# Optimization experiments

Hardware: AMD Instinct MI355X
Metric: run time of the kernel (lower is better)

Reference implementation:

```python
import jax, jax.numpy as jnp
import numpy as np

N, FIN, H, C, D = 50000, 128, 4, 64, 4
E = 800000


def leaky_relu(x, slope):
    return jnp.where(x >= 0, x, slope * x)


def gat_layer(x, src, dst, W, A, att_src, att_dst, bias):
    # x: [N, Fin]; W: [Fin, H*C]; A: [Fin, H*D]; att_*: [H, D]; bias: [C]
    n = x.shape[0]
    h = (x @ W).reshape(n, H, -1)          # [N, H, C] message features
    a = (x @ A).reshape(n, H, -1)          # [N, H, D] attention features
    alpha_src = jnp.einsum('nhd,hd->nh', a, att_src)   # [N, H]
    alpha_dst = jnp.einsum('nhd,hd->nh', a, att_dst)   # [N, H]
    e = leaky_relu(alpha_src[src] + alpha_dst[dst], 0.2)  # [E, H]
    # edge softmax over incoming edges of each destination node
    m = jax.ops.segment_max(e, dst, num_segments=n)       # [N, H]
    ex = jnp.exp(e - m[dst])                               # [E, H]
    denom = jax.ops.segment_sum(ex, dst, num_segments=n)  # [N, H]
    w = ex / denom[dst]                                    # [E, H]
    msg = h[src] * w[..., None]                            # [E, H, C]
    out = jax.ops.segment_sum(msg, dst, num_segments=n)   # [N, H, C]
    return out.mean(axis=1) + bias                         # head-average -> [N, C]


def setup_inputs() -> dict:
    key = jax.random.key(0)
    ks = jax.random.split(key, 12)
    x = jax.random.normal(ks[0], (N, FIN), dtype=jnp.float32)
    edge_index = jax.random.randint(ks[1], (2, E), 0, N, dtype=jnp.int64)
    s = 0.05
    return {
        'x': x,
        'edge_index': edge_index,
        'W1': jax.random.normal(ks[2], (FIN, H * C), dtype=jnp.float32) * s,
        'A1': jax.random.normal(ks[3], (FIN, H * D), dtype=jnp.float32) * s,
        'att_src1': jax.random.normal(ks[4], (H, D), dtype=jnp.float32) * s,
        'att_dst1': jax.random.normal(ks[5], (H, D), dtype=jnp.float32) * s,
        'b1': jnp.zeros((C,), dtype=jnp.float32),
        'W2': jax.random.normal(ks[6], (C, H * C), dtype=jnp.float32) * s,
        'A2': jax.random.normal(ks[7], (C, H * D), dtype=jnp.float32) * s,
        'att_src2': jax.random.normal(ks[8], (H, D), dtype=jnp.float32) * s,
        'att_dst2': jax.random.normal(ks[9], (H, D), dtype=jnp.float32) * s,
        'b2': jnp.zeros((C,), dtype=jnp.float32),
    }


def reference(x, edge_index, W1, A1, att_src1, att_dst1, b1, W2, A2, att_src2, att_dst2, b2):
    src, dst = edge_index[0], edge_index[1]
    x = gat_layer(x, src, dst, W1, A1, att_src1, att_dst1, b1)
    x = leaky_relu(x, 0.1)
    x = gat_layer(x, src, dst, W2, A2, att_src2, att_dst2, b2)
    x = leaky_relu(x, 0.1)
    return x
```

## Files before the change

### kernel.cpp

```cpp
#include <hip/hip_runtime.h>


#define N_NODES 50000
#define N_EDGES 800000
#define NB_EDGE 3125
#define CAP 64

typedef _Float16 half4 __attribute__((ext_vector_type(4)));
typedef __attribute__((ext_vector_type(8))) short short8;
typedef __attribute__((ext_vector_type(4))) float f32x4;
typedef __attribute__((ext_vector_type(8))) unsigned short ushort8;

__device__ __forceinline__ float bf2f(unsigned short u){
  return __uint_as_float(((unsigned int)u) << 16);
}
__device__ __forceinline__ unsigned short f2bf(float f){
  unsigned int u = __float_as_uint(f);
  u = (u + 0x7FFFu + ((u >> 16) & 1u)) >> 16;
  return (unsigned short)u;
}
__device__ __forceinline__ float ldf(const void* p, int i, bool bf){
  return bf ? bf2f(((const unsigned short*)p)[i]) : ((const float*)p)[i];
}

struct SetupPtrs {
  const void *W1, *A1, *aS1, *aD1, *b1, *W2, *A2, *aS2, *aD2, *b2, *x;
};

__global__ __launch_bounds__(256) void k_setup(SetupPtrs S,
    unsigned short* __restrict__ Wb1, unsigned short* __restrict__ Wb2,
    unsigned short* __restrict__ Bsd1f, unsigned short* __restrict__ Bsd2f,
    float* __restrict__ bc1, float* __restrict__ bc2,
    int* __restrict__ flag)
{
  __shared__ int sbf;
  const int tid = threadIdx.x;
  if (tid < 64){
    unsigned int w = ((const unsigned int*)S.x)[tid] & 0xFFFFu;
    unsigned int e = (w >> 7) & 0xFFu;
    bool hit = (e >= 100u && e <= 135u);
    unsigned long long m = __ballot(hit);
    if (tid == 0) sbf = (__popcll(m) > 40) ? 1 : 0;
  }
  __syncthreads();
  const bool bf = (sbf != 0);
  const int bw = blockIdx.x;
  if (bw < 128){
    int t = bw * 256 + tid;
    int j = t & 7, lane = (t >> 3) & 63, kt = (t >> 9) & 3, nt = t >> 11;
    int k = kt * 32 + (lane >> 4) * 8 + j;
    int n = nt * 16 + (lane & 15);
    Wb1[t] = bf ? ((const unsigned short*)S.W1)[k * 256 + n]
                : f2bf(((const float*)S.W1)[k * 256 + n]);
  } else if (bw < 192){
    int t = (bw - 128) * 256 + tid;
    int j = t & 7, lane = (t >> 3) & 63, kt = (t >> 9) & 1, nt = t >> 10;
    int k = kt * 32 + (lane >> 4) * 8 + j;
    int n = nt * 16 + (lane & 15);
    Wb2[t] = bf ? ((const unsigned short*)S.W2)[k * 256 + n]
                : f2bf(((const float*)S.W2)[k * 256 + n]);
  } else if (bw < 200){
    int t = (bw - 192) * 256 + tid;
    int j = t & 7, lane = (t >> 3) & 63, kt = t >> 9;
    int k = kt * 32 + (lane >> 4) * 8 + j;
    int c = lane & 15;
    float v = 0.f;
    if (c < 4){
      for (int dd = 0; dd < 4; ++dd)
        v += ldf(S.A1, k * 16 + c * 4 + dd, bf) * ldf(S.aS1, c * 4 + dd, bf);
    } else if (c < 8){
      int h = c - 4;
      for (int dd = 0; dd < 4; ++dd)
        v += ldf(S.A1, k * 16 + h * 4 + dd, bf) * ldf(S.aD1, h * 4 + dd, bf);
    }
    Bsd1f[t] = f2bf(v);
  } else if (bw < 204){
    int t = (bw - 200) * 256 + tid;
    int j = t & 7, lane = (t >> 3) & 63, kt = t >> 9;
    int k = kt * 32 + (lane >> 4) * 8 + j;
    int c = lane & 15;
    float v = 0.f;
    if (c < 4){
      for (int dd = 0; dd < 4; ++dd)
        v += ldf(S.A2, k * 16 + c * 4 + dd, bf) * ldf(S.aS2, c * 4 + dd, bf);
    } else if (c < 8){
      int h = c - 4;
      for (int dd = 0; dd < 4; ++dd)
        v += ldf(S.A2, k * 16 + h * 4 + dd, bf) * ldf(S.aD2, h * 4 + dd, bf);
    }
    Bsd2f[t] = f2bf(v);
  } else {
    if (tid < 64)       bc1[tid] = ldf(S.b1, tid, bf);
    else if (tid < 128) bc2[tid - 64] = ldf(S.b2, tid - 64, bf);
    else if (tid == 128) *flag = bf ? 1 : 0;
  }
}


template<int F, bool DYN>
__device__ __forceinline__ void nodeM_body(int nblk, int tid,
    const void* __restrict__ xin_,
    const unsigned short* __restrict__ Wb, const unsigned short* __restrict__ Bsdf,
    _Float16* __restrict__ hmat, float* __restrict__ alpha_s, float* __restrict__ alpha_d,
    const int* __restrict__ flag)
{
  const int STR = F + 8;
  const int KT  = F / 32;
  const int CH  = F / 8;
  __shared__ unsigned short xs[64 * (F + 8)];
  const int base = nblk * 64;
  bool bf = true;
  if (DYN) bf = (*flag != 0);
  for (int v = tid; v < 64 * CH; v += 256){
    int row = v / CH, c8 = v % CH;
    int node = base + row; if (node >= N_NODES) node = N_NODES - 1;
    size_t g = (size_t)node * F + c8 * 8;
    ushort8 u;
    if (!DYN || bf){
      u = *(const ushort8*)((const unsigned short*)xin_ + g);
    } else {
      const float* xf = (const float*)xin_ + g;
      float4 f0 = *(const float4*)xf, f1 = *(const float4*)(xf + 4);
      u[0]=f2bf(f0.x); u[1]=f2bf(f0.y); u[2]=f2bf(f0.z); u[3]=f2bf(f0.w);
      u[4]=f2bf(f1.x); u[5]=f2bf(f1.y); u[6]=f2bf(f1.z); u[7]=f2bf(f1.w);
    }
    *(ushort8*)&xs[row * STR + c8 * 8] = u;
  }
  __syncthreads();

  const int wave = tid >> 6, l = tid & 63;
  const int quad = l >> 4, m = l & 15;
  const int wbase = base + wave * 16;

  short8 afrag[KT];
  #pragma unroll
  for (int kt = 0; kt < KT; ++kt)
    afrag[kt] = *(const short8*)&xs[(wave * 16 + m) * STR + kt * 32 + quad * 8];

  f32x4 aacc = (f32x4)0.f;
  #pragma unroll
  for (int kt = 0; kt < KT; ++kt){
    short8 sdfrag = *(const short8*)(Bsdf + ((size_t)kt * 64 + l) * 8);
    aacc = __builtin_amdgcn_mfma_f32_16x16x32_bf16(afrag[kt], sdfrag, aacc, 0, 0, 0);
  }
  if (m < 8){
    float* dstp = (m < 4) ? alpha_s : alpha_d;
    int hh = m & 3;
    #pragma unroll
    for (int r = 0; r < 4; ++r){
      int node = wbase + quad * 4 + r;
      if (node < N_NODES) dstp[node * 4 + hh] = aacc[r];
    }
  }

  f32x4 acc[16];
  #pragma unroll
  for (int nt = 0; nt < 16; ++nt) acc[nt] = (f32x4)0.f;

  #pragma unroll
  for (int nt = 0; nt < 16; ++nt){
    #pragma unroll
    for (int kt = 0; kt < KT; ++kt){
      short8 bfrag = *(const short8*)(Wb + ((size_t)(nt * KT + kt) * 64 + l) * 8);
      acc[nt] = __builtin_amdgcn_mfma_f32_16x16x32_bf16(afrag[kt], bfrag, acc[nt], 0, 0, 0);
    }
  }
  #pragma unroll
  for (int r = 0; r < 4; ++r){
    int node = wbase + quad * 4 + r;
    if (node < N_NODES){
      #pragma unroll
      for (int nt = 0; nt < 16; ++nt)
        hmat[(size_t)node * 256 + nt * 16 + m] = (_Float16)acc[nt][r];
    }
  }
}


__global__ __launch_bounds__(256) void k_scatter_node1(
    const int* __restrict__ src, const int* __restrict__ dst,
    int* __restrict__ fill, int* __restrict__ csr_src,
    const void* __restrict__ xin_,
    const unsigned short* __restrict__ Wb, const unsigned short* __restrict__ Bsdf,
    _Float16* __restrict__ hmat, float* __restrict__ alpha_s, float* __restrict__ alpha_d,
    const int* __restrict__ flag)
{
  const int b = blockIdx.x, tid = threadIdx.x;
  if (b < NB_EDGE){
    int e = b * 256 + tid;
    int d = dst[e];
    int r = atomicAdd(&fill[d], 1);
    if (r < CAP) csr_src[(d << 6) + r] = src[e];
    return;
  }
  nodeM_body<128, true>(b - NB_EDGE, tid, xin_, Wb, Bsdf, hmat, alpha_s, alpha_d, flag);
}

template<int F, bool DYN>
__global__ __launch_bounds__(256) void k_nodeM(const void* __restrict__ xin_,
    const unsigned short* __restrict__ Wb, const unsigned short* __restrict__ Bsdf,
    _Float16* __restrict__ hmat, float* __restrict__ alpha_s, float* __restrict__ alpha_d,
    const int* __restrict__ flag)
{
  nodeM_body<F, DYN>(blockIdx.x, threadIdx.x, xin_, Wb, Bsdf, hmat, alpha_s, alpha_d, flag);
}


template<int MODE>
__global__ __launch_bounds__(256) void k_aggr(
    const _Float16* __restrict__ hmat, const float* __restrict__ alpha_s,
    const float* __restrict__ alpha_d, const int* __restrict__ fill,
    const int* __restrict__ csr_src, const float* __restrict__ bias,
    void* __restrict__ out, const int* __restrict__ flag)
{
  const int tid = threadIdx.x;
  const int wave = tid >> 6, l = tid & 63;
  const int n = blockIdx.x * 4 + wave;
  const int hh = l >> 4;
  const float adv = alpha_d[n * 4 + hh];
  int cnt = fill[n]; if (cnt > CAP) cnt = CAP;
  const int p0 = n << 6, p1 = p0 + cnt;
  const char* hb = (const char*)hmat + l * 8;
  const char* ab = (const char*)alpha_s + hh * 4;
  float4 acc = make_float4(0.f,0.f,0.f,0.f);
  float den = 0.f;
  int p = p0;
  for (; p + 4 <= p1; p += 4){
    int4 s4 = *(const int4*)(csr_src + p);
    float a0 = *(const float*)(ab + ((unsigned)s4.x << 4));
    float a1 = *(const float*)(ab + ((unsigned)s4.y << 4));
    float a2 = *(const float*)(ab + ((unsigned)s4.z << 4));
    float a3 = *(const float*)(ab + ((unsigned)s4.w << 4));
    half4 h0 = *(const half4*)(hb + ((unsigned)s4.x << 9));
    half4 h1 = *(const half4*)(hb + ((unsigned)s4.y << 9));
    half4 h2 = *(const half4*)(hb + ((unsigned)s4.z << 9));
    half4 h3 = *(const half4*)(hb + ((unsigned)s4.w << 9));
    float e0 = a0 + adv; e0 = fmaxf(e0, 0.2f * e0);
    float e1 = a1 + adv; e1 = fmaxf(e1, 0.2f * e1);
    float e2 = a2 + adv; e2 = fmaxf(e2, 0.2f * e2);
    float e3 = a3 + adv; e3 = fmaxf(e3, 0.2f * e3);
    float ex0 = __expf(e0), ex1 = __expf(e1), ex2 = __expf(e2), ex3 = __expf(e3);
    den += (ex0 + ex1) + (ex2 + ex3);
    acc.x += ex0 * (float)h0.x + ex1 * (float)h1.x + ex2 * (float)h2.x + ex3 * (float)h3.x;
    acc.y += ex0 * (float)h0.y + ex1 * (float)h1.y + ex2 * (float)h2.y + ex3 * (float)h3.y;
    acc.z += ex0 * (float)h0.z + ex1 * (float)h1.z + ex2 * (float)h2.z + ex3 * (float)h3.z;
    acc.w += ex0 * (float)h0.w + ex1 * (float)h1.w + ex2 * (float)h2.w + ex3 * (float)h3.w;
  }
  for (; p < p1; ++p){
    int s = csr_src[p];
    float e = *(const float*)(ab + ((unsigned)s << 4)) + adv;
    e = fmaxf(e, 0.2f * e);
    float ex = __expf(e);
    half4 hv = *(const half4*)(hb + ((unsigned)s << 9));
    den += ex;
    acc.x += ex * (float)hv.x; acc.y += ex * (float)hv.y;
    acc.z += ex * (float)hv.z; acc.w += ex * (float)hv.w;
  }
  float r = (den > 0.f) ? (1.f / den) : 0.f;
  acc.x *= r; acc.y *= r; acc.z *= r; acc.w *= r;
  acc.x += __shfl_xor(acc.x, 16); acc.y += __shfl_xor(acc.y, 16);
  acc.z += __shfl_xor(acc.z, 16); acc.w += __shfl_xor(acc.w, 16);
  acc.x += __shfl_xor(acc.x, 32); acc.y += __shfl_xor(acc.y, 32);
  acc.z += __shfl_xor(acc.z, 32); acc.w += __shfl_xor(acc.w, 32);
  if (l < 16){
    float vx = 0.25f * acc.x + bias[l * 4 + 0];
    float vy = 0.25f * acc.y + bias[l * 4 + 1];
    float vz = 0.25f * acc.z + bias[l * 4 + 2];
    float vw = 0.25f * acc.w + bias[l * 4 + 3];
    vx = fmaxf(vx, 0.1f * vx);
    vy = fmaxf(vy, 0.1f * vy);
    vz = fmaxf(vz, 0.1f * vz);
    vw = fmaxf(vw, 0.1f * vw);
    if (MODE == 0){
      ushort4 o = make_ushort4(f2bf(vx), f2bf(vy), f2bf(vz), f2bf(vw));
      *(ushort4*)((unsigned short*)out + (size_t)n * 64 + l * 4) = o;
    } else {
      if (*flag){
        ushort4 o = make_ushort4(f2bf(vx), f2bf(vy), f2bf(vz), f2bf(vw));
        *(ushort4*)((unsigned short*)out + (size_t)n * 64 + l * 4) = o;
      } else {
        *(float4*)((float*)out + (size_t)n * 64 + l * 4) = make_float4(vx, vy, vz, vw);
      }
    }
  }
}


extern "C" void kernel_launch(void* const* d_in, const int* in_sizes, int n_in,
                              void* d_out, int out_size, void* d_ws, size_t ws_size,
                              hipStream_t stream)
{
  const void* x  = d_in[0];
  const int* ei  = (const int*)d_in[1];
  const int* src = ei;
  const int* dst = ei + N_EDGES;

  char* ws = (char*)d_ws;
  _Float16* hmat = (_Float16*)(ws);
  int*   csr    = (int*)  (ws + 25600000);
  unsigned short* x2  = (unsigned short*)(ws + 38400000);
  float* as_    = (float*)(ws + 44800000);
  float* ad_    = (float*)(ws + 45600000);
  int*   fill   = (int*)  (ws + 46400000);
  unsigned short* Wb1 = (unsigned short*)(ws + 46600000);
  unsigned short* Wb2 = (unsigned short*)(ws + 46665536);
  unsigned short* Bsd1f = (unsigned short*)(ws + 46698304);
  unsigned short* Bsd2f = (unsigned short*)(ws + 46702400);
  float* bc1    = (float*)(ws + 46704448);
  float* bc2    = (float*)(ws + 46704704);
  int*   flag   = (int*)  (ws + 46704960);

  hipMemsetAsync(fill, 0, N_NODES * sizeof(int), stream);

  SetupPtrs S;
  S.W1 = d_in[2];  S.A1 = d_in[3];  S.aS1 = d_in[4];  S.aD1 = d_in[5];  S.b1 = d_in[6];
  S.W2 = d_in[7];  S.A2 = d_in[8];  S.aS2 = d_in[9];  S.aD2 = d_in[10]; S.b2 = d_in[11];
  S.x  = x;
  k_setup<<<205, 256, 0, stream>>>(S, Wb1, Wb2, Bsd1f, Bsd2f, bc1, bc2, flag);

  k_scatter_node1<<<NB_EDGE + (N_NODES + 63) / 64, 256, 0, stream>>>(
      src, dst, fill, csr, x, Wb1, Bsd1f, hmat, as_, ad_, flag);

  k_aggr<0><<<N_NODES / 4, 256, 0, stream>>>(hmat, as_, ad_, fill, csr, bc1, x2, flag);
  k_nodeM<64, false><<<(N_NODES + 63) / 64, 256, 0, stream>>>(x2, Wb2, Bsd2f, hmat, as_, ad_, flag);
  k_aggr<1><<<N_NODES / 4, 256, 0, stream>>>(hmat, as_, ad_, fill, csr, bc2, d_out, flag);
}
```

Before: 298.9 us.

## Aggregate raw features before projection, then apply per-head weights via MFMA

Reorders each GAT layer so edge-softmax aggregation runs on the input features x (per head) and the W projection, with the head mean folded into the weights, is applied afterward in an f16 MFMA over the aggregated [4*Fin] rows. This removes the 256-wide h matrix write and its per-edge gather, replacing it with gathers of narrower x rows. CSR source indices are also stored as 16-bit, and edge scatter handles four edges per thread. The cost is per-edge work for all four heads per lane, an extra LDS staging step and some f16 rounding of the aggregated values.

```diff
diff --git a/kernel.cpp b/kernel.cpp
--- a/kernel.cpp
+++ b/kernel.cpp
@@ -3,11 +3,12 @@
 
 #define N_NODES 50000
 #define N_EDGES 800000
-#define NB_EDGE 3125
 #define CAP 64
-
-typedef _Float16 half4 __attribute__((ext_vector_type(4)));
+#define NB_SC4 782
+#define NB_NODE1 782
+
 typedef __attribute__((ext_vector_type(8))) short short8;
+typedef __attribute__((ext_vector_type(8))) _Float16 f16x8;
 typedef __attribute__((ext_vector_type(4))) float f32x4;
 typedef __attribute__((ext_vector_type(8))) unsigned short ushort8;
 
@@ -28,7 +29,7 @@
 };
 
 __global__ __launch_bounds__(256) void k_setup(SetupPtrs S,
-    unsigned short* __restrict__ Wb1, unsigned short* __restrict__ Wb2,
+    _Float16* __restrict__ Wb1f, _Float16* __restrict__ Wb2f,
     unsigned short* __restrict__ Bsd1f, unsigned short* __restrict__ Bsd2f,
     float* __restrict__ bc1, float* __restrict__ bc2,
     int* __restrict__ flag)
@@ -47,18 +48,18 @@
   const int bw = blockIdx.x;
   if (bw < 128){
     int t = bw * 256 + tid;
-    int j = t & 7, lane = (t >> 3) & 63, kt = (t >> 9) & 3, nt = t >> 11;
-    int k = kt * 32 + (lane >> 4) * 8 + j;
-    int n = nt * 16 + (lane & 15);
-    Wb1[t] = bf ? ((const unsigned short*)S.W1)[k * 256 + n]
-                : f2bf(((const float*)S.W1)[k * 256 + n]);
+    int j = t & 7, lane = (t >> 3) & 63, kt = (t >> 9) & 15, nt = t >> 13;
+    int q = kt * 32 + (lane >> 4) * 8 + j;
+    int c = nt * 16 + (lane & 15);
+    int h = q >> 7, f = q & 127;
+    Wb1f[t] = (_Float16)(0.25f * ldf(S.W1, f * 256 + h * 64 + c, bf));
   } else if (bw < 192){
     int t = (bw - 128) * 256 + tid;
-    int j = t & 7, lane = (t >> 3) & 63, kt = (t >> 9) & 1, nt = t >> 10;
-    int k = kt * 32 + (lane >> 4) * 8 + j;
-    int n = nt * 16 + (lane & 15);
-    Wb2[t] = bf ? ((const unsigned short*)S.W2)[k * 256 + n]
-                : f2bf(((const float*)S.W2)[k * 256 + n]);
+    int j = t & 7, lane = (t >> 3) & 63, kt = (t >> 9) & 7, nt = t >> 12;
+    int q = kt * 32 + (lane >> 4) * 8 + j;
+    int c = nt * 16 + (lane & 15);
+    int h = q >> 6, f = q & 63;
+    Wb2f[t] = (_Float16)(0.25f * ldf(S.W2, f * 256 + h * 64 + c, bf));
   } else if (bw < 200){
     int t = (bw - 192) * 256 + tid;
     int j = t & 7, lane = (t >> 3) & 63, kt = t >> 9;
@@ -98,10 +99,9 @@
 
 
 template<int F, bool DYN>
-__device__ __forceinline__ void nodeM_body(int nblk, int tid,
-    const void* __restrict__ xin_,
-    const unsigned short* __restrict__ Wb, const unsigned short* __restrict__ Bsdf,
-    _Float16* __restrict__ hmat, float* __restrict__ alpha_s, float* __restrict__ alpha_d,
+__device__ __forceinline__ void nodeA_body(int nblk, int tid,
+    const void* __restrict__ xin_, const unsigned short* __restrict__ Bsdf,
+    float* __restrict__ alpha_s, float* __restrict__ alpha_d,
     const int* __restrict__ flag)
 {
   const int STR = F + 8;
@@ -132,16 +132,12 @@
   const int quad = l >> 4, m = l & 15;
   const int wbase = base + wave * 16;
 
-  short8 afrag[KT];
-  #pragma unroll
-  for (int kt = 0; kt < KT; ++kt)
-    afrag[kt] = *(const short8*)&xs[(wave * 16 + m) * STR + kt * 32 + quad * 8];
-
   f32x4 aacc = (f32x4)0.f;
   #pragma unroll
   for (int kt = 0; kt < KT; ++kt){
+    short8 af = *(const short8*)&xs[(wave * 16 + m) * STR + kt * 32 + quad * 8];
     short8 sdfrag = *(const short8*)(Bsdf + ((size_t)kt * 64 + l) * 8);
-    aacc = __builtin_amdgcn_mfma_f32_16x16x32_bf16(afrag[kt], sdfrag, aacc, 0, 0, 0);
+    aacc = __builtin_amdgcn_mfma_f32_16x16x32_bf16(af, sdfrag, aacc, 0, 0, 0);
   }
   if (m < 8){
     float* dstp = (m < 4) ? alpha_s : alpha_d;
@@ -152,135 +148,173 @@
       if (node < N_NODES) dstp[node * 4 + hh] = aacc[r];
     }
   }
-
-  f32x4 acc[16];
+}
+
+
+__global__ __launch_bounds__(256) void k_scatter_nodeA1(
+    const int* __restrict__ src, const int* __restrict__ dst,
+    int* __restrict__ fill, unsigned short* __restrict__ csr,
+    const void* __restrict__ xin_, const unsigned short* __restrict__ Bsdf,
+    float* __restrict__ alpha_s, float* __restrict__ alpha_d,
+    const int* __restrict__ flag)
+{
+  const int b = blockIdx.x, tid = threadIdx.x;
+  if (b < NB_SC4){
+    const int ebase = b * 1024 + tid;
+    int d[4], s[4];
+    #pragma unroll
+    for (int i = 0; i < 4; ++i){
+      int e = ebase + i * 256;
+      bool ok = (e < N_EDGES);
+      d[i] = ok ? dst[e] : -1;
+      s[i] = ok ? src[e] : 0;
+    }
+    #pragma unroll
+    for (int i = 0; i < 4; ++i){
+      if (d[i] >= 0){
+        int r = atomicAdd(&fill[d[i]], 1);
+        if (r < CAP) csr[((unsigned)d[i] << 6) + r] = (unsigned short)s[i];
+      }
+    }
+    return;
+  }
+  nodeA_body<128, true>(b - NB_SC4, tid, xin_, Bsdf, alpha_s, alpha_d, flag);
+}
+
+template<int F, bool DYN>
+__global__ __launch_bounds__(256) void k_nodeA(const void* __restrict__ xin_,
+    const unsigned short* __restrict__ Bsdf,
+    float* __restrict__ alpha_s, float* __restrict__ alpha_d,
+    const int* __restrict__ flag)
+{
+  nodeA_body<F, DYN>(blockIdx.x, threadIdx.x, xin_, Bsdf, alpha_s, alpha_d, flag);
+}
+
+
+template<int NF>
+__device__ __forceinline__ void edge_acc(unsigned int xv, const float4 as4,
+    const float4 ad4, float den[4], float acc[4][NF])
+{
+  float e0 = as4.x + ad4.x; e0 = fmaxf(e0, 0.2f * e0); float w0 = __expf(e0);
+  float e1 = as4.y + ad4.y; e1 = fmaxf(e1, 0.2f * e1); float w1 = __expf(e1);
+  float e2 = as4.z + ad4.z; e2 = fmaxf(e2, 0.2f * e2); float w2 = __expf(e2);
+  float e3 = as4.w + ad4.w; e3 = fmaxf(e3, 0.2f * e3); float w3 = __expf(e3);
+  den[0] += w0; den[1] += w1; den[2] += w2; den[3] += w3;
+  float lo = bf2f((unsigned short)(xv & 0xFFFFu));
+  acc[0][0] += w0 * lo; acc[1][0] += w1 * lo;
+  acc[2][0] += w2 * lo; acc[3][0] += w3 * lo;
+  if (NF == 2){
+    float hi = bf2f((unsigned short)(xv >> 16));
+    acc[0][NF-1] += w0 * hi; acc[1][NF-1] += w1 * hi;
+    acc[2][NF-1] += w2 * hi; acc[3][NF-1] += w3 * hi;
+  }
+}
+
+template<int FIN, bool BF>
+__device__ __forceinline__ unsigned int ldx(const void* xg, unsigned s, int l){
+  if (FIN == 128){
+    if (BF) return *(const unsigned int*)((const unsigned short*)xg + (size_t)s * 128 + 2 * l);
+    const float* xf = (const float*)xg + (size_t)s * 128 + 2 * l;
+    return (unsigned int)f2bf(xf[0]) | ((unsigned int)f2bf(xf[1]) << 16);
+  } else {
+    if (BF) return (unsigned int)((const unsigned short*)xg)[(size_t)s * 64 + l];
+    return (unsigned int)f2bf(((const float*)xg)[(size_t)s * 64 + l]);
+  }
+}
+
+template<int FIN, bool BF, int NF, int STR>
+__device__ __forceinline__ void aggr_phase1(const void* __restrict__ xg,
+    const float* __restrict__ alpha_s, const float* __restrict__ alpha_d,
+    const int* __restrict__ fill, const unsigned short* __restrict__ csr,
+    _Float16* __restrict__ ylds, int base, int w, int l)
+{
+  #pragma unroll 1
+  for (int r = 0; r < 4; ++r){
+    const int n = base + w * 4 + r;
+    const float4 ad4 = *(const float4*)(alpha_d + n * 4);
+    float den[4] = {0.f, 0.f, 0.f, 0.f};
+    float acc[4][NF];
+    #pragma unroll
+    for (int h = 0; h < 4; ++h)
+      #pragma unroll
+      for (int f = 0; f < NF; ++f) acc[h][f] = 0.f;
+
+    int cnt = fill[n]; if (cnt > CAP) cnt = CAP;
+    const unsigned short* cp = csr + ((unsigned)n << 6);
+    int p = 0;
+    for (; p + 4 <= cnt; p += 4){
+      ushort4 s4 = *(const ushort4*)(cp + p);
+      const float4 a0 = *(const float4*)(alpha_s + s4.x * 4);
+      const float4 a1 = *(const float4*)(alpha_s + s4.y * 4);
+      const float4 a2 = *(const float4*)(alpha_s + s4.z * 4);
+      const float4 a3 = *(const float4*)(alpha_s + s4.w * 4);
+      unsigned int v0 = ldx<FIN, BF>(xg, s4.x, l);
+      unsigned int v1 = ldx<FIN, BF>(xg, s4.y, l);
+      unsigned int v2 = ldx<FIN, BF>(xg, s4.z, l);
+      unsigned int v3 = ldx<FIN, BF>(xg, s4.w, l);
+      edge_acc<NF>(v0, a0, ad4, den, acc);
+      edge_acc<NF>(v1, a1, ad4, den, acc);
+      edge_acc<NF>(v2, a2, ad4, den, acc);
+      edge_acc<NF>(v3, a3, ad4, den, acc);
+    }
+    for (; p < cnt; ++p){
+      unsigned s = cp[p];
+      const float4 a0 = *(const float4*)(alpha_s + s * 4);
+      unsigned int v0 = ldx<FIN, BF>(xg, s, l);
+      edge_acc<NF>(v0, a0, ad4, den, acc);
+    }
+    const int row = w * 4 + r;
+    #pragma unroll
+    for (int h = 0; h < 4; ++h){
+      float rh = (den[h] > 0.f) ? (1.f / den[h]) : 0.f;
+      #pragma unroll
+      for (int f = 0; f < NF; ++f)
+        ylds[row * STR + h * FIN + NF * l + f] = (_Float16)(acc[h][f] * rh);
+    }
+  }
+}
+
+template<int FIN, int MODE>
+__global__ __launch_bounds__(256) void k_aggrX(
+    const void* __restrict__ xg,
+    const float* __restrict__ alpha_s, const float* __restrict__ alpha_d,
+    const int* __restrict__ fill, const unsigned short* __restrict__ csr,
+    const _Float16* __restrict__ Wf,
+    const float* __restrict__ bias, void* __restrict__ out,
+    const int* __restrict__ flag)
+{
+  const int K = 4 * FIN, KT = K / 32, STR = K + 8, NF = FIN / 64;
+  __shared__ _Float16 ylds[16 * (4 * FIN + 8)];
+  const int tid = threadIdx.x, w = tid >> 6, l = tid & 63;
+  const int base = blockIdx.x * 16;
+
+  if (MODE == 0 && *flag == 0)
+    aggr_phase1<FIN, false, NF, STR>(xg, alpha_s, alpha_d, fill, csr, ylds, base, w, l);
+  else
+    aggr_phase1<FIN, true,  NF, STR>(xg, alpha_s, alpha_d, fill, csr, ylds, base, w, l);
+  __syncthreads();
+
+  const int quad = l >> 4, m = l & 15;
+  const int nt = w;
+  f32x4 cacc = (f32x4)0.f;
   #pragma unroll
-  for (int nt = 0; nt < 16; ++nt) acc[nt] = (f32x4)0.f;
-
+  for (int kt = 0; kt < KT; ++kt){
+    f16x8 av = *(const f16x8*)&ylds[m * STR + kt * 32 + quad * 8];
+    f16x8 bv = *(const f16x8*)(Wf + ((size_t)(nt * KT + kt) * 64 + l) * 8);
+    cacc = __builtin_amdgcn_mfma_f32_16x16x32_f16(av, bv, cacc, 0, 0, 0);
+  }
+  const int c = nt * 16 + m;
+  const float bs = bias[c];
   #pragma unroll
-  for (int nt = 0; nt < 16; ++nt){
-    #pragma unroll
-    for (int kt = 0; kt < KT; ++kt){
-      short8 bfrag = *(const short8*)(Wb + ((size_t)(nt * KT + kt) * 64 + l) * 8);
-      acc[nt] = __builtin_amdgcn_mfma_f32_16x16x32_bf16(afrag[kt], bfrag, acc[nt], 0, 0, 0);
-    }
-  }
-  #pragma unroll
-  for (int r = 0; r < 4; ++r){
-    int node = wbase + quad * 4 + r;
-    if (node < N_NODES){
-      #pragma unroll
-      for (int nt = 0; nt < 16; ++nt)
-        hmat[(size_t)node * 256 + nt * 16 + m] = (_Float16)acc[nt][r];
-    }
-  }
-}
-
-
-__global__ __launch_bounds__(256) void k_scatter_node1(
-    const int* __restrict__ src, const int* __restrict__ dst,
-    int* __restrict__ fill, int* __restrict__ csr_src,
-    const void* __restrict__ xin_,
-    const unsigned short* __restrict__ Wb, const unsigned short* __restrict__ Bsdf,
-    _Float16* __restrict__ hmat, float* __restrict__ alpha_s, float* __restrict__ alpha_d,
-    const int* __restrict__ flag)
-{
-  const int b = blockIdx.x, tid = threadIdx.x;
-  if (b < NB_EDGE){
-    int e = b * 256 + tid;
-    int d = dst[e];
-    int r = atomicAdd(&fill[d], 1);
-    if (r < CAP) csr_src[(d << 6) + r] = src[e];
-    return;
-  }
-  nodeM_body<128, true>(b - NB_EDGE, tid, xin_, Wb, Bsdf, hmat, alpha_s, alpha_d, flag);
-}
-
-template<int F, bool DYN>
-__global__ __launch_bounds__(256) void k_nodeM(const void* __restrict__ xin_,
-    const unsigned short* __restrict__ Wb, const unsigned short* __restrict__ Bsdf,
-    _Float16* __restrict__ hmat, float* __restrict__ alpha_s, float* __restrict__ alpha_d,
-    const int* __restrict__ flag)
-{
-  nodeM_body<F, DYN>(blockIdx.x, threadIdx.x, xin_, Wb, Bsdf, hmat, alpha_s, alpha_d, flag);
-}
-
-
-template<int MODE>
-__global__ __launch_bounds__(256) void k_aggr(
-    const _Float16* __restrict__ hmat, const float* __restrict__ alpha_s,
-    const float* __restrict__ alpha_d, const int* __restrict__ fill,
-    const int* __restrict__ csr_src, const float* __restrict__ bias,
-    void* __restrict__ out, const int* __restrict__ flag)
-{
-  const int tid = threadIdx.x;
-  const int wave = tid >> 6, l = tid & 63;
-  const int n = blockIdx.x * 4 + wave;
-  const int hh = l >> 4;
-  const float adv = alpha_d[n * 4 + hh];
-  int cnt = fill[n]; if (cnt > CAP) cnt = CAP;
-  const int p0 = n << 6, p1 = p0 + cnt;
-  const char* hb = (const char*)hmat + l * 8;
-  const char* ab = (const char*)alpha_s + hh * 4;
-  float4 acc = make_float4(0.f,0.f,0.f,0.f);
-  float den = 0.f;
-  int p = p0;
-  for (; p + 4 <= p1; p += 4){
-    int4 s4 = *(const int4*)(csr_src + p);
-    float a0 = *(const float*)(ab + ((unsigned)s4.x << 4));
-    float a1 = *(const float*)(ab + ((unsigned)s4.y << 4));
-    float a2 = *(const float*)(ab + ((unsigned)s4.z << 4));
-    float a3 = *(const float*)(ab + ((unsigned)s4.w << 4));
-    half4 h0 = *(const half4*)(hb + ((unsigned)s4.x << 9));
-    half4 h1 = *(const half4*)(hb + ((unsigned)s4.y << 9));
-    half4 h2 = *(const half4*)(hb + ((unsigned)s4.z << 9));
-    half4 h3 = *(const half4*)(hb + ((unsigned)s4.w << 9));
-    float e0 = a0 + adv; e0 = fmaxf(e0, 0.2f * e0);
-    float e1 = a1 + adv; e1 = fmaxf(e1, 0.2f * e1);
-    float e2 = a2 + adv; e2 = fmaxf(e2, 0.2f * e2);
-    float e3 = a3 + adv; e3 = fmaxf(e3, 0.2f * e3);
-    float ex0 = __expf(e0), ex1 = __expf(e1), ex2 = __expf(e2), ex3 = __expf(e3);
-    den += (ex0 + ex1) + (ex2 + ex3);
-    acc.x += ex0 * (float)h0.x + ex1 * (float)h1.x + ex2 * (float)h2.x + ex3 * (float)h3.x;
-    acc.y += ex0 * (float)h0.y + ex1 * (float)h1.y + ex2 * (float)h2.y + ex3 * (float)h3.y;
-    acc.z += ex0 * (float)h0.z + ex1 * (float)h1.z + ex2 * (float)h2.z + ex3 * (float)h3.z;
-    acc.w += ex0 * (float)h0.w + ex1 * (float)h1.w + ex2 * (float)h2.w + ex3 * (float)h3.w;
-  }
-  for (; p < p1; ++p){
-    int s = csr_src[p];
-    float e = *(const float*)(ab + ((unsigned)s << 4)) + adv;
-    e = fmaxf(e, 0.2f * e);
-    float ex = __expf(e);
-    half4 hv = *(const half4*)(hb + ((unsigned)s << 9));
-    den += ex;
-    acc.x += ex * (float)hv.x; acc.y += ex * (float)hv.y;
-    acc.z += ex * (float)hv.z; acc.w += ex * (float)hv.w;
-  }
-  float r = (den > 0.f) ? (1.f / den) : 0.f;
-  acc.x *= r; acc.y *= r; acc.z *= r; acc.w *= r;
-  acc.x += __shfl_xor(acc.x, 16); acc.y += __shfl_xor(acc.y, 16);
-  acc.z += __shfl_xor(acc.z, 16); acc.w += __shfl_xor(acc.w, 16);
-  acc.x += __shfl_xor(acc.x, 32); acc.y += __shfl_xor(acc.y, 32);
-  acc.z += __shfl_xor(acc.z, 32); acc.w += __shfl_xor(acc.w, 32);
-  if (l < 16){
-    float vx = 0.25f * acc.x + bias[l * 4 + 0];
-    float vy = 0.25f * acc.y + bias[l * 4 + 1];
-    float vz = 0.25f * acc.z + bias[l * 4 + 2];
-    float vw = 0.25f * acc.w + bias[l * 4 + 3];
-    vx = fmaxf(vx, 0.1f * vx);
-    vy = fmaxf(vy, 0.1f * vy);
-    vz = fmaxf(vz, 0.1f * vz);
-    vw = fmaxf(vw, 0.1f * vw);
+  for (int r2 = 0; r2 < 4; ++r2){
+    int node = base + quad * 4 + r2;
+    float v = cacc[r2] + bs;
+    v = fmaxf(v, 0.1f * v);
     if (MODE == 0){
-      ushort4 o = make_ushort4(f2bf(vx), f2bf(vy), f2bf(vz), f2bf(vw));
-      *(ushort4*)((unsigned short*)out + (size_t)n * 64 + l * 4) = o;
+      ((unsigned short*)out)[(size_t)node * 64 + c] = f2bf(v);
     } else {
-      if (*flag){
-        ushort4 o = make_ushort4(f2bf(vx), f2bf(vy), f2bf(vz), f2bf(vw));
-        *(ushort4*)((unsigned short*)out + (size_t)n * 64 + l * 4) = o;
-      } else {
-        *(float4*)((float*)out + (size_t)n * 64 + l * 4) = make_float4(vx, vy, vz, vw);
-      }
+      if (*flag) ((unsigned short*)out)[(size_t)node * 64 + c] = f2bf(v);
+      else       ((float*)out)[(size_t)node * 64 + c] = v;
     }
   }
 }
@@ -296,19 +330,18 @@
   const int* dst = ei + N_EDGES;
 
   char* ws = (char*)d_ws;
-  _Float16* hmat = (_Float16*)(ws);
-  int*   csr    = (int*)  (ws + 25600000);
-  unsigned short* x2  = (unsigned short*)(ws + 38400000);
-  float* as_    = (float*)(ws + 44800000);
-  float* ad_    = (float*)(ws + 45600000);
-  int*   fill   = (int*)  (ws + 46400000);
-  unsigned short* Wb1 = (unsigned short*)(ws + 46600000);
-  unsigned short* Wb2 = (unsigned short*)(ws + 46665536);
-  unsigned short* Bsd1f = (unsigned short*)(ws + 46698304);
-  unsigned short* Bsd2f = (unsigned short*)(ws + 46702400);
-  float* bc1    = (float*)(ws + 46704448);
-  float* bc2    = (float*)(ws + 46704704);
-  int*   flag   = (int*)  (ws + 46704960);
+  unsigned short* csr = (unsigned short*)(ws);
+  unsigned short* x2  = (unsigned short*)(ws + 6400000);
+  float* as_    = (float*)(ws + 12800000);
+  float* ad_    = (float*)(ws + 13600000);
+  int*   fill   = (int*)  (ws + 14400000);
+  _Float16* Wb1f = (_Float16*)(ws + 14600000);
+  _Float16* Wb2f = (_Float16*)(ws + 14665536);
+  unsigned short* Bsd1f = (unsigned short*)(ws + 14698304);
+  unsigned short* Bsd2f = (unsigned short*)(ws + 14702400);
+  float* bc1    = (float*)(ws + 14704448);
+  float* bc2    = (float*)(ws + 14704704);
+  int*   flag   = (int*)  (ws + 14704960);
 
   hipMemsetAsync(fill, 0, N_NODES * sizeof(int), stream);
 
@@ -316,12 +349,16 @@
   S.W1 = d_in[2];  S.A1 = d_in[3];  S.aS1 = d_in[4];  S.aD1 = d_in[5];  S.b1 = d_in[6];
   S.W2 = d_in[7];  S.A2 = d_in[8];  S.aS2 = d_in[9];  S.aD2 = d_in[10]; S.b2 = d_in[11];
   S.x  = x;
-  k_setup<<<205, 256, 0, stream>>>(S, Wb1, Wb2, Bsd1f, Bsd2f, bc1, bc2, flag);
-
-  k_scatter_node1<<<NB_EDGE + (N_NODES + 63) / 64, 256, 0, stream>>>(
-      src, dst, fill, csr, x, Wb1, Bsd1f, hmat, as_, ad_, flag);
-
-  k_aggr<0><<<N_NODES / 4, 256, 0, stream>>>(hmat, as_, ad_, fill, csr, bc1, x2, flag);
-  k_nodeM<64, false><<<(N_NODES + 63) / 64, 256, 0, stream>>>(x2, Wb2, Bsd2f, hmat, as_, ad_, flag);
-  k_aggr<1><<<N_NODES / 4, 256, 0, stream>>>(hmat, as_, ad_, fill, csr, bc2, d_out, flag);
-}
+  k_setup<<<205, 256, 0, stream>>>(S, Wb1f, Wb2f, Bsd1f, Bsd2f, bc1, bc2, flag);
+
+  k_scatter_nodeA1<<<NB_SC4 + NB_NODE1, 256, 0, stream>>>(
+      src, dst, fill, csr, x, Bsd1f, as_, ad_, flag);
+
+  k_aggrX<128, 0><<<N_NODES / 16, 256, 0, stream>>>(
+      x, as_, ad_, fill, csr, Wb1f, bc1, x2, flag);
+
+  k_nodeA<64, false><<<NB_NODE1, 256, 0, stream>>>(x2, Bsd2f, as_, ad_, flag);
+
+  k_aggrX<64, 1><<<N_NODES / 16, 256, 0, stream>>>(
+      x2, as_, ad_, fill, csr, Wb2f, bc2, d_out, flag);
+}
```

Result: slower. 322.1 us (+7.8%).
